# Performance work log

Measured on AMD Instinct MI355X. Metric: run time of the kernel, lower is better.

## Reference

```python
import jax, jax.numpy as jnp
import numpy as np

EMBED_DIM = 1024
NUM_HEADS = 16
HEAD_DIM = EMBED_DIM // NUM_HEADS
MAX_REL = 64
B, S = 4, 1024


def setup_inputs() -> dict:
    key = jax.random.key(0)
    ks = jax.random.split(key, 12)
    scale = 1.0 / np.sqrt(EMBED_DIM)
    inp = {
        "query": jax.random.normal(ks[0], (B, S, EMBED_DIM), jnp.float32),
        "key": jax.random.normal(ks[1], (B, S, EMBED_DIM), jnp.float32),
        "value": jax.random.normal(ks[2], (B, S, EMBED_DIM), jnp.float32),
        "attn_mask": jnp.ones((B, 1, S, S), jnp.int32),
        # projection weights stored [in, out] so x @ W matches torch Linear(x) with W = weight.T
        "Wq": jax.random.normal(ks[3], (EMBED_DIM, EMBED_DIM), jnp.float32) * scale,
        "bq": jnp.zeros((EMBED_DIM,), jnp.float32),
        "Wk": jax.random.normal(ks[4], (EMBED_DIM, EMBED_DIM), jnp.float32) * scale,
        "bk": jnp.zeros((EMBED_DIM,), jnp.float32),
        "Wv": jax.random.normal(ks[5], (EMBED_DIM, EMBED_DIM), jnp.float32) * scale,
        "bv": jnp.zeros((EMBED_DIM,), jnp.float32),
        "Wo": jax.random.normal(ks[6], (EMBED_DIM, EMBED_DIM), jnp.float32) * scale,
        "bo": jnp.zeros((EMBED_DIM,), jnp.float32),
        "rel_pos_embed": jax.random.normal(ks[7], (2 * MAX_REL + 1, HEAD_DIM), jnp.float32) * 0.02,
    }
    return inp


def _split_heads(x):
    # [B, S, E] -> [B, H, S, D]
    b, s, _ = x.shape
    return x.reshape(b, s, NUM_HEADS, HEAD_DIM).transpose(0, 2, 1, 3)


def reference(query, key, value, attn_mask, Wq, bq, Wk, bk, Wv, bv, Wo, bo, rel_pos_embed):
    q = _split_heads(query @ Wq + bq)
    k = _split_heads(key @ Wk + bk)
    v = _split_heads(value @ Wv + bv)

    scores = jnp.einsum("bhqd,bhkd->bhqk", q, k) / np.sqrt(HEAD_DIM).astype(np.float32)

    # relative position bias: rel_pos[i, j] = rel_pos_embed[clip(i - j) + MAX_REL]
    seq_len = scores.shape[-1]
    rng = jnp.arange(seq_len)
    range_mat = jnp.clip(rng[:, None] - rng[None, :], -MAX_REL, MAX_REL) + MAX_REL
    rel_pos = rel_pos_embed[range_mat]                       # [S, S, D]
    # torch: matmul(q[...,None,:], rel_pos.mT).squeeze(-2) == einsum over head_dim (NOT scaled)
    rel_scores = jnp.einsum("bhid,ijd->bhij", q, rel_pos)
    scores = scores + rel_scores

    scores = jnp.where(attn_mask == 0, -jnp.inf, scores)
    attn_weights = jax.nn.softmax(scores, axis=-1)           # dropout p=0.0 -> identity

    out = jnp.einsum("bhqk,bhkd->bhqd", attn_weights, v)
    out = out.transpose(0, 2, 1, 3).reshape(query.shape[0], -1, EMBED_DIM)
    out = out @ Wo + bo
    return out, attn_weights
```

## Files before the change

kernel.cpp:

```cpp
#include <hip/hip_runtime.h>
#include <math.h>

#define BB 4
#define SS 1024
#define EE 1024
#define HH 16
#define DD 64
#define RR 129
#define PRELW 130

typedef __attribute__((ext_vector_type(4))) float f32x4;
typedef __attribute__((ext_vector_type(4))) int   i32x4;
typedef __attribute__((ext_vector_type(8))) short bf8;
typedef __attribute__((ext_vector_type(4))) short s4v;

#define MFMA(a, b, c) __builtin_amdgcn_mfma_f32_16x16x32_bf16(a, b, c, 0, 0, 0)

__device__ __forceinline__ float bf2f(unsigned short u) {
    return __uint_as_float(((unsigned)u) << 16);
}
__device__ __forceinline__ unsigned short f2bf(float x) {
    unsigned u = __float_as_uint(x);
    return (unsigned short)((u + 0x7fffu + ((u >> 16) & 1u)) >> 16);
}

__global__ __launch_bounds__(256, 4)
void wtrans_kernel(const float* __restrict__ Wq, const float* __restrict__ Wk,
                   const float* __restrict__ Wv, const float* __restrict__ Wo,
                   unsigned short* __restrict__ wt_hi, unsigned short* __restrict__ wt_lo)
{
    __shared__ float T[64][65];
    const int w = blockIdx.z;
    const float* W = w == 0 ? Wq : (w == 1 ? Wk : (w == 2 ? Wv : Wo));
    const int n0 = blockIdx.x * 64, k0 = blockIdx.y * 64;
    const int tid = threadIdx.x;
#pragma unroll
    for (int i = 0; i < 4; ++i) {
        int c = tid + 256 * i; int r = c >> 4, c4 = c & 15;
        f32x4 v = *(const f32x4*)(W + (size_t)(k0 + r) * EE + n0 + c4 * 4);
        T[r][c4 * 4 + 0] = v.x; T[r][c4 * 4 + 1] = v.y;
        T[r][c4 * 4 + 2] = v.z; T[r][c4 * 4 + 3] = v.w;
    }
    __syncthreads();
#pragma unroll
    for (int i = 0; i < 4; ++i) {
        int c = tid + 256 * i; int r = c >> 4, c4 = c & 15;
        float x0 = T[c4 * 4 + 0][r], x1 = T[c4 * 4 + 1][r];
        float x2 = T[c4 * 4 + 2][r], x3 = T[c4 * 4 + 3][r];
        unsigned short h0 = f2bf(x0), h1 = f2bf(x1), h2 = f2bf(x2), h3 = f2bf(x3);
        unsigned short l0 = f2bf(x0 - bf2f(h0)), l1 = f2bf(x1 - bf2f(h1));
        unsigned short l2 = f2bf(x2 - bf2f(h2)), l3 = f2bf(x3 - bf2f(h3));
        size_t o = (size_t)w * 1048576 + (size_t)(n0 + r) * 1024 + k0 + c4 * 4;
        *(s4v*)&wt_hi[o] = (s4v){(short)h0, (short)h1, (short)h2, (short)h3};
        *(s4v*)&wt_lo[o] = (s4v){(short)l0, (short)l1, (short)l2, (short)l3};
    }
}

__global__ __launch_bounds__(256)
void maskbits_kernel(const int* __restrict__ mask, unsigned long long* __restrict__ mb)
{
    const int w = blockIdx.x * 256 + threadIdx.x;
    const int* p = mask + (size_t)w * 64;
    unsigned long long bits = 0;
#pragma unroll
    for (int i = 0; i < 16; ++i) {
        int4 v = *(const int4*)(p + i * 4);
        bits |= (unsigned long long)(v.x != 0) << (i * 4 + 0);
        bits |= (unsigned long long)(v.y != 0) << (i * 4 + 1);
        bits |= (unsigned long long)(v.z != 0) << (i * 4 + 2);
        bits |= (unsigned long long)(v.w != 0) << (i * 4 + 3);
    }
    mb[w] = bits;
}

template<int ASRC, int EPI>
__device__ __forceinline__ void gemm_body(
    const float* __restrict__ Af,
    const unsigned short* __restrict__ Ah_g, const unsigned short* __restrict__ Al_g,
    const unsigned short* __restrict__ Bh_g, const unsigned short* __restrict__ Bl_g,
    const float* __restrict__ bias,
    float* __restrict__ Yf, unsigned short* __restrict__ Yh, unsigned short* __restrict__ Yl,
    unsigned short* As_h, unsigned short* As_l, unsigned short* Bs_h, unsigned short* Bs_l,
    int m0, int n0)
{
    const int tid = threadIdx.x, lane = tid & 63, wid = tid >> 6;
    const int wm = (wid >> 1) * 64, wn = (wid & 1) * 64;
    f32x4 zero4 = {0.f, 0.f, 0.f, 0.f};
    f32x4 acc[4][4];
#pragma unroll
    for (int a = 0; a < 4; ++a)
#pragma unroll
        for (int b = 0; b < 4; ++b) acc[a][b] = zero4;

    for (int kt = 0; kt < 1024; kt += 64) {
        __syncthreads();
        if (ASRC == 0) {
#pragma unroll
            for (int i = 0; i < 8; ++i) {
                int c = tid + 256 * i; int r = c >> 4, c4 = c & 15;
                f32x4 v = *(const f32x4*)(Af + (size_t)(m0 + r) * 1024 + kt + c4 * 4);
                unsigned short h0 = f2bf(v.x), h1 = f2bf(v.y), h2 = f2bf(v.z), h3 = f2bf(v.w);
                unsigned short l0 = f2bf(v.x - bf2f(h0)), l1 = f2bf(v.y - bf2f(h1));
                unsigned short l2 = f2bf(v.z - bf2f(h2)), l3 = f2bf(v.w - bf2f(h3));
                int off = r * 64 + (((c4 >> 1) ^ (r & 7)) * 8) + (c4 & 1) * 4;
                *(s4v*)&As_h[off] = (s4v){(short)h0, (short)h1, (short)h2, (short)h3};
                *(s4v*)&As_l[off] = (s4v){(short)l0, (short)l1, (short)l2, (short)l3};
            }
        } else {
#pragma unroll
            for (int i = 0; i < 4; ++i) {
                int c = tid + 256 * i; int r = c >> 3, cc = c & 7;
                int off = r * 64 + ((cc ^ (r & 7)) * 8);
                *(bf8*)&As_h[off] = *(const bf8*)(Ah_g + (size_t)(m0 + r) * 1024 + kt + cc * 8);
                *(bf8*)&As_l[off] = *(const bf8*)(Al_g + (size_t)(m0 + r) * 1024 + kt + cc * 8);
            }
        }
#pragma unroll
        for (int i = 0; i < 4; ++i) {
            int c = tid + 256 * i; int r = c >> 3, cc = c & 7;
            int off = r * 64 + ((cc ^ (r & 7)) * 8);
            *(bf8*)&Bs_h[off] = *(const bf8*)(Bh_g + (size_t)(n0 + r) * 1024 + kt + cc * 8);
            *(bf8*)&Bs_l[off] = *(const bf8*)(Bl_g + (size_t)(n0 + r) * 1024 + kt + cc * 8);
        }
        __syncthreads();
#pragma unroll
        for (int ks = 0; ks < 2; ++ks) {
            bf8 ah[4], al[4], bh[4], bl[4];
#pragma unroll
            for (int f = 0; f < 4; ++f) {
                int ra = wm + f * 16 + (lane & 15);
                int ca = (ks * 4 + (lane >> 4)) ^ (ra & 7);
                ah[f] = *(const bf8*)&As_h[ra * 64 + ca * 8];
                al[f] = *(const bf8*)&As_l[ra * 64 + ca * 8];
                int rb = wn + f * 16 + (lane & 15);
                int cb = (ks * 4 + (lane >> 4)) ^ (rb & 7);
                bh[f] = *(const bf8*)&Bs_h[rb * 64 + cb * 8];
                bl[f] = *(const bf8*)&Bs_l[rb * 64 + cb * 8];
            }
#pragma unroll
            for (int fi = 0; fi < 4; ++fi)
#pragma unroll
                for (int fj = 0; fj < 4; ++fj) {
                    acc[fi][fj] = MFMA(ah[fi], bh[fj], acc[fi][fj]);
                    acc[fi][fj] = MFMA(al[fi], bh[fj], acc[fi][fj]);
                    acc[fi][fj] = MFMA(ah[fi], bl[fj], acc[fi][fj]);
                }
        }
    }
#pragma unroll
    for (int fi = 0; fi < 4; ++fi)
#pragma unroll
        for (int fj = 0; fj < 4; ++fj)
#pragma unroll
            for (int rg = 0; rg < 4; ++rg) {
                int m = m0 + wm + fi * 16 + ((lane >> 4) << 2) + rg;
                int n = n0 + wn + fj * 16 + (lane & 15);
                float val = acc[fi][fj][rg] + bias[n];
                if (EPI == 0) {
                    int b = m >> 10, s = m & 1023, h = n >> 6, d = n & 63;
                    size_t o = (((size_t)(b * 16 + h)) * 1024 + s) * 64 + d;
                    unsigned short hv = f2bf(val);
                    unsigned short lv = f2bf(val - bf2f(hv));
                    Yh[o] = hv; Yl[o] = lv;
                } else {
                    Yf[(size_t)m * 1024 + n] = val;
                }
            }
}

__global__ __launch_bounds__(256, 2)
void proj_qkv_kernel(const float* __restrict__ q_in, const float* __restrict__ k_in,
                     const float* __restrict__ v_in,
                     const unsigned short* __restrict__ wt_hi, const unsigned short* __restrict__ wt_lo,
                     const float* __restrict__ bq, const float* __restrict__ bk,
                     const float* __restrict__ bv,
                     unsigned short* qh_hi, unsigned short* qh_lo,
                     unsigned short* kh_hi, unsigned short* kh_lo,
                     unsigned short* vh_hi, unsigned short* vh_lo)
{
    __shared__ __align__(16) unsigned short As_h[128 * 64], As_l[128 * 64];
    __shared__ __align__(16) unsigned short Bs_h[128 * 64], Bs_l[128 * 64];
    const int z = blockIdx.z;
    const float* X = z == 0 ? q_in : (z == 1 ? k_in : v_in);
    const float* bias = z == 0 ? bq : (z == 1 ? bk : bv);
    unsigned short* Yh = z == 0 ? qh_hi : (z == 1 ? kh_hi : vh_hi);
    unsigned short* Yl = z == 0 ? qh_lo : (z == 1 ? kh_lo : vh_lo);
    gemm_body<0, 0>(X, nullptr, nullptr,
                    wt_hi + (size_t)z * 1048576, wt_lo + (size_t)z * 1048576,
                    bias, nullptr, Yh, Yl, As_h, As_l, Bs_h, Bs_l,
                    blockIdx.x * 128, blockIdx.y * 128);
}

__global__ __launch_bounds__(256, 2)
void outproj_kernel(const unsigned short* __restrict__ ctx_hi, const unsigned short* __restrict__ ctx_lo,
                    const unsigned short* __restrict__ wo_hi, const unsigned short* __restrict__ wo_lo,
                    const float* __restrict__ bo, float* __restrict__ out)
{
    __shared__ __align__(16) unsigned short As_h[128 * 64], As_l[128 * 64];
    __shared__ __align__(16) unsigned short Bs_h[128 * 64], Bs_l[128 * 64];
    gemm_body<1, 1>(nullptr, ctx_hi, ctx_lo, wo_hi, wo_lo, bo, out, nullptr, nullptr,
                    As_h, As_l, Bs_h, Bs_l, blockIdx.x * 128, blockIdx.y * 128);
}

__global__ __launch_bounds__(256, 4)
void vtrans_kernel(const unsigned short* __restrict__ vh_hi, const unsigned short* __restrict__ vh_lo,
                   unsigned short* __restrict__ vt_hi, unsigned short* __restrict__ vt_lo)
{
    __shared__ unsigned short T[64][72];
    const unsigned short* src = blockIdx.z ? vh_lo : vh_hi;
    unsigned short* dst = blockIdx.z ? vt_lo : vt_hi;
    const int st = blockIdx.x * 64, bh = blockIdx.y, tid = threadIdx.x;
#pragma unroll
    for (int i = 0; i < 4; ++i) {
        int c = tid + 256 * i; int r = c >> 4, d4 = c & 15;
        s4v v = *(const s4v*)(src + ((size_t)bh * 1024 + st + r) * 64 + d4 * 4);
        T[r][d4 * 4 + 0] = (unsigned short)v.x; T[r][d4 * 4 + 1] = (unsigned short)v.y;
        T[r][d4 * 4 + 2] = (unsigned short)v.z; T[r][d4 * 4 + 3] = (unsigned short)v.w;
    }
    __syncthreads();
#pragma unroll
    for (int i = 0; i < 4; ++i) {
        int c = tid + 256 * i; int r = c >> 4, s4_ = c & 15;
        s4v o = {(short)T[s4_ * 4 + 0][r], (short)T[s4_ * 4 + 1][r],
                 (short)T[s4_ * 4 + 2][r], (short)T[s4_ * 4 + 3][r]};
        *(s4v*)(dst + ((size_t)bh * 64 + r) * 1024 + st + s4_ * 4) = o;
    }
}

__global__ __launch_bounds__(256, 2)
void attn_fused_kernel(const unsigned short* __restrict__ qh_hi, const unsigned short* __restrict__ qh_lo,
                       const unsigned short* __restrict__ kh_hi, const unsigned short* __restrict__ kh_lo,
                       const unsigned short* __restrict__ vt_hi, const unsigned short* __restrict__ vt_lo,
                       const float* __restrict__ emb, const unsigned long long* __restrict__ mb,
                       float* __restrict__ attn,
                       unsigned short* __restrict__ ctx_hi, unsigned short* __restrict__ ctx_lo)
{
    __shared__ __align__(16) unsigned short Sh[128 * 64], Sl[128 * 64];
    __shared__ __align__(16) unsigned short Pr[128 * PRELW];
    __shared__ float Sm[2][128], Ss[2][128], SmF[128], SsF[128];
    const int tid = threadIdx.x, lane = tid & 63, wid = tid >> 6;
    const int wi = wid >> 1, wj = wid & 1;
    const int g = lane >> 4, li = lane & 15;
    const int bh = blockIdx.x, i0 = blockIdx.y * 128, b = bh >> 4;
    const f32x4 zero4 = {0.f, 0.f, 0.f, 0.f};

    const unsigned short* qbh = qh_hi + ((size_t)bh * 1024 + i0) * 64;
    const unsigned short* qbl = qh_lo + ((size_t)bh * 1024 + i0) * 64;
#pragma unroll
    for (int i = 0; i < 4; ++i) {
        int c = tid + 256 * i; int r = c >> 3, cc = c & 7;
        int off = r * 64 + ((cc ^ (r & 7)) * 8);
        *(bf8*)&Sh[off] = *(const bf8*)(qbh + r * 64 + cc * 8);
        *(bf8*)&Sl[off] = *(const bf8*)(qbl + r * 64 + cc * 8);
    }
    __syncthreads();

    bf8 qfh[4][2], qfl[4][2];
#pragma unroll
    for (int fi = 0; fi < 4; ++fi)
#pragma unroll
        for (int ks = 0; ks < 2; ++ks) {
            int rb = wi * 64 + fi * 16 + li;
            int cb = (ks * 4 + g) ^ (rb & 7);
            qfh[fi][ks] = *(const bf8*)&Sh[rb * 64 + cb * 8];
            qfl[fi][ks] = *(const bf8*)&Sl[rb * 64 + cb * 8];
        }

    for (int t = wid; t < 72; t += 4) {
        const int it = t / 9, rt = t % 9;
        f32x4 pc = zero4;
#pragma unroll
        for (int ks = 0; ks < 2; ++ks) {
            int ra = it * 16 + li;
            int ca = (ks * 4 + g) ^ (ra & 7);
            bf8 aq = *(const bf8*)&Sh[ra * 64 + ca * 8];
            int er = rt * 16 + li; if (er > 128) er = 128;
            const float* ep = emb + (size_t)er * 64 + ks * 32 + g * 8;
            f32x4 e0 = *(const f32x4*)ep;
            f32x4 e1 = *(const f32x4*)(ep + 4);
            bf8 be = {(short)f2bf(e0.x), (short)f2bf(e0.y), (short)f2bf(e0.z), (short)f2bf(e0.w),
                      (short)f2bf(e1.x), (short)f2bf(e1.y), (short)f2bf(e1.z), (short)f2bf(e1.w)};
            pc = MFMA(aq, be, pc);
        }
        const int rcol = rt * 16 + li;
        if (rcol < RR) {
#pragma unroll
            for (int rg = 0; rg < 4; ++rg)
                Pr[(it * 16 + g * 4 + rg) * PRELW + rcol] = f2bf(pc[rg]);
        }
    }

    float rm[4], rs[4];
#pragma unroll
    for (int i = 0; i < 4; ++i) { rm[i] = -3.0e38f; rs[i] = 0.f; }

    for (int jt = 0; jt < 8; ++jt) {
        __syncthreads();
        const unsigned short* kbh = kh_hi + ((size_t)bh * 1024 + jt * 128) * 64;
        const unsigned short* kbl = kh_lo + ((size_t)bh * 1024 + jt * 128) * 64;
#pragma unroll
        for (int i = 0; i < 4; ++i) {
            int c = tid + 256 * i; int r = c >> 3, cc = c & 7;
            int off = r * 64 + ((cc ^ (r & 7)) * 8);
            *(bf8*)&Sh[off] = *(const bf8*)(kbh + r * 64 + cc * 8);
            *(bf8*)&Sl[off] = *(const bf8*)(kbl + r * 64 + cc * 8);
        }
        __syncthreads();
        f32x4 acc[4][4];
#pragma unroll
        for (int a = 0; a < 4; ++a)
#pragma unroll
            for (int c = 0; c < 4; ++c) acc[a][c] = zero4;
#pragma unroll
        for (int ks = 0; ks < 2; ++ks) {
            bf8 kfh[4], kfl[4];
#pragma unroll
            for (int fj = 0; fj < 4; ++fj) {
                int ra = wj * 64 + fj * 16 + li;
                int ca = (ks * 4 + g) ^ (ra & 7);
                kfh[fj] = *(const bf8*)&Sh[ra * 64 + ca * 8];
                kfl[fj] = *(const bf8*)&Sl[ra * 64 + ca * 8];
            }
#pragma unroll
            for (int fj = 0; fj < 4; ++fj)
#pragma unroll
                for (int fi = 0; fi < 4; ++fi) {
                    acc[fj][fi] = MFMA(kfh[fj], qfh[fi][ks], acc[fj][fi]);
                    acc[fj][fi] = MFMA(kfl[fj], qfh[fi][ks], acc[fj][fi]);
                    acc[fj][fi] = MFMA(kfh[fj], qfl[fi][ks], acc[fj][fi]);
                }
        }
#pragma unroll
        for (int fi = 0; fi < 4; ++fi) {
            const int rowL = wi * 64 + fi * 16 + li;
            const int ii = i0 + rowL;
            const unsigned long long mw = mb[((size_t)b * 1024 + ii) * 16 + jt * 2 + wj];
            float p16[4][4];
            float tmax = -3.0e38f;
#pragma unroll
            for (int fj = 0; fj < 4; ++fj)
#pragma unroll
                for (int rg = 0; rg < 4; ++rg) {
                    int jloc = fj * 16 + g * 4 + rg;
                    int jj = jt * 128 + wj * 64 + jloc;
                    int dd = ii - jj; dd = dd < -64 ? -64 : (dd > 64 ? 64 : dd);
                    float s = acc[fj][fi][rg] * 0.125f + bf2f(Pr[rowL * PRELW + dd + 64]);
                    if (!((mw >> jloc) & 1ull)) s = -1.0e30f;
                    p16[fj][rg] = s;
                    tmax = fmaxf(tmax, s);
                }
            tmax = fmaxf(tmax, __shfl_xor(tmax, 16, 64));
            tmax = fmaxf(tmax, __shfl_xor(tmax, 32, 64));
            float nm = fmaxf(rm[fi], tmax);
            float ps = 0.f;
#pragma unroll
            for (int fj = 0; fj < 4; ++fj)
#pragma unroll
                for (int rg = 0; rg < 4; ++rg) ps += __expf(p16[fj][rg] - nm);
            ps += __shfl_xor(ps, 16, 64);
            ps += __shfl_xor(ps, 32, 64);
            rs[fi] = rs[fi] * __expf(rm[fi] - nm) + ps;
            rm[fi] = nm;
        }
    }
#pragma unroll
    for (int fi = 0; fi < 4; ++fi) {
        if (lane < 16) {
            Sm[wj][wi * 64 + fi * 16 + li] = rm[fi];
            Ss[wj][wi * 64 + fi * 16 + li] = rs[fi];
        }
    }
    __syncthreads();
    if (tid < 128) {
        float m0_ = Sm[0][tid], m1_ = Sm[1][tid];
        float mmx = fmaxf(m0_, m1_);
        SmF[tid] = mmx;
        SsF[tid] = Ss[0][tid] * __expf(m0_ - mmx) + Ss[1][tid] * __expf(m1_ - mmx);
    }
    __syncthreads();
    float mm4[4], iv4[4];
#pragma unroll
    for (int fi = 0; fi < 4; ++fi) {
        mm4[fi] = SmF[wi * 64 + fi * 16 + li];
        iv4[fi] = 1.f / SsF[wi * 64 + fi * 16 + li];
    }

    f32x4 ctx_acc[4][4];
#pragma unroll
    for (int a = 0; a < 4; ++a)
#pragma unroll
        for (int c = 0; c < 4; ++c) ctx_acc[a][c] = zero4;

    for (int jt = 0; jt < 8; ++jt) {
        __syncthreads();
        const unsigned short* kbh = kh_hi + ((size_t)bh * 1024 + jt * 128) * 64;
        const unsigned short* kbl = kh_lo + ((size_t)bh * 1024 + jt * 128) * 64;
#pragma unroll
        for (int i = 0; i < 4; ++i) {
            int c = tid + 256 * i; int r = c >> 3, cc = c & 7;
            int off = r * 64 + ((cc ^ (r & 7)) * 8);
            *(bf8*)&Sh[off] = *(const bf8*)(kbh + r * 64 + cc * 8);
            *(bf8*)&Sl[off] = *(const bf8*)(kbl + r * 64 + cc * 8);
        }
        __syncthreads();
        f32x4 acc[4][4];
#pragma unroll
        for (int a = 0; a < 4; ++a)
#pragma unroll
            for (int c = 0; c < 4; ++c) acc[a][c] = zero4;
#pragma unroll
        for (int ks = 0; ks < 2; ++ks) {
            bf8 kfh[4], kfl[4];
#pragma unroll
            for (int fj = 0; fj < 4; ++fj) {
                int ra = wj * 64 + fj * 16 + li;
                int ca = (ks * 4 + g) ^ (ra & 7);
                kfh[fj] = *(const bf8*)&Sh[ra * 64 + ca * 8];
                kfl[fj] = *(const bf8*)&Sl[ra * 64 + ca * 8];
            }
#pragma unroll
            for (int fj = 0; fj < 4; ++fj)
#pragma unroll
                for (int fi = 0; fi < 4; ++fi) {
                    acc[fj][fi] = MFMA(kfh[fj], qfh[fi][ks], acc[fj][fi]);
                    acc[fj][fi] = MFMA(kfl[fj], qfh[fi][ks], acc[fj][fi]);
                    acc[fj][fi] = MFMA(kfh[fj], qfl[fi][ks], acc[fj][fi]);
                }
        }
#pragma unroll
        for (int c = 0; c < 2; ++c) {
            bf8 vfh[4], vfl[4];
#pragma unroll
            for (int fd = 0; fd < 4; ++fd) {
                size_t vb = (size_t)bh * 65536 + (size_t)(fd * 16 + li) * 1024
                          + jt * 128 + wj * 64 + c * 32 + g * 8;
                vfh[fd] = *(const bf8*)(vt_hi + vb);
                vfl[fd] = *(const bf8*)(vt_lo + vb);
            }
#pragma unroll
            for (int fi = 0; fi < 4; ++fi) {
                const int rowL = wi * 64 + fi * 16 + li;
                const int ii = i0 + rowL;
                const unsigned long long mw = mb[((size_t)b * 1024 + ii) * 16 + jt * 2 + wj];
                const float mmf = mm4[fi], ivf = iv4[fi];
                float* arow = attn + ((size_t)bh * 1024 + ii) * 1024 + jt * 128 + wj * 64 + g * 4;
                unsigned wh[2][2], wl[2][2];
#pragma unroll
                for (int t = 0; t < 2; ++t) {
                    const int fj = c * 2 + t;
                    f32x4 pv;
#pragma unroll
                    for (int rg = 0; rg < 4; ++rg) {
                        int jloc = fj * 16 + g * 4 + rg;
                        int jj = jt * 128 + wj * 64 + jloc;
                        int dd = ii - jj; dd = dd < -64 ? -64 : (dd > 64 ? 64 : dd);
                        float s = acc[fj][fi][rg] * 0.125f + bf2f(Pr[rowL * PRELW + dd + 64]);
                        if (!((mw >> jloc) & 1ull)) s = -1.0e30f;
                        pv[rg] = __expf(s - mmf) * ivf;
                    }
                    __builtin_nontemporal_store(pv, (f32x4*)(arow + fj * 16));
                    unsigned short h0 = f2bf(pv.x), h1 = f2bf(pv.y), h2 = f2bf(pv.z), h3 = f2bf(pv.w);
                    wh[t][0] = (unsigned)h0 | ((unsigned)h1 << 16);
                    wh[t][1] = (unsigned)h2 | ((unsigned)h3 << 16);
                    unsigned short l0 = f2bf(pv.x - bf2f(h0)), l1 = f2bf(pv.y - bf2f(h1));
                    unsigned short l2 = f2bf(pv.z - bf2f(h2)), l3 = f2bf(pv.w - bf2f(h3));
                    wl[t][0] = (unsigned)l0 | ((unsigned)l1 << 16);
                    wl[t][1] = (unsigned)l2 | ((unsigned)l3 << 16);
                }
                const int src0 = ((g & 1) * 2) * 16 + li;
                const int src1 = src0 + 16;
                const bool hiT = (g >> 1) & 1;
                int x0A = __shfl((int)wh[0][0], src0, 64), x0B = __shfl((int)wh[1][0], src0, 64);
                int x1A = __shfl((int)wh[0][1], src0, 64), x1B = __shfl((int)wh[1][1], src0, 64);
                int x2A = __shfl((int)wh[0][0], src1, 64), x2B = __shfl((int)wh[1][0], src1, 64);
                int x3A = __shfl((int)wh[0][1], src1, 64), x3B = __shfl((int)wh[1][1], src1, 64);
                i32x4 awh = {hiT ? x0B : x0A, hiT ? x1B : x1A, hiT ? x2B : x2A, hiT ? x3B : x3A};
                bf8 pah = *(bf8*)&awh;
                int y0A = __shfl((int)wl[0][0], src0, 64), y0B = __shfl((int)wl[1][0], src0, 64);
                int y1A = __shfl((int)wl[0][1], src0, 64), y1B = __shfl((int)wl[1][1], src0, 64);
                int y2A = __shfl((int)wl[0][0], src1, 64), y2B = __shfl((int)wl[1][0], src1, 64);
                int y3A = __shfl((int)wl[0][1], src1, 64), y3B = __shfl((int)wl[1][1], src1, 64);
                i32x4 awl = {hiT ? y0B : y0A, hiT ? y1B : y1A, hiT ? y2B : y2A, hiT ? y3B : y3A};
                bf8 pal = *(bf8*)&awl;
#pragma unroll
                for (int fd = 0; fd < 4; ++fd) {
                    ctx_acc[fi][fd] = MFMA(pah, vfh[fd], ctx_acc[fi][fd]);
                    ctx_acc[fi][fd] = MFMA(pal, vfh[fd], ctx_acc[fi][fd]);
                    ctx_acc[fi][fd] = MFMA(pah, vfl[fd], ctx_acc[fi][fd]);
                }
            }
        }
    }

    __syncthreads();
    float* red = (wi == 0) ? (float*)Sh : (float*)Sl;
    if (wj == 1) {
#pragma unroll
        for (int fi = 0; fi < 4; ++fi)
#pragma unroll
            for (int fd = 0; fd < 4; ++fd)
#pragma unroll
                for (int rg = 0; rg < 4; ++rg) {
                    int idx = (fi * 4 + fd) * 4 + rg;
                    red[lane * 64 + ((idx + lane) & 63)] = ctx_acc[fi][fd][rg];
                }
    }
    __syncthreads();
    if (wj == 0) {
        const int b_ = bh >> 4, h = bh & 15;
#pragma unroll
        for (int fi = 0; fi < 4; ++fi)
#pragma unroll
            for (int fd = 0; fd < 4; ++fd)
#pragma unroll
                for (int rg = 0; rg < 4; ++rg) {
                    int idx = (fi * 4 + fd) * 4 + rg;
                    float val = ctx_acc[fi][fd][rg] + red[lane * 64 + ((idx + lane) & 63)];
                    int ii = i0 + wi * 64 + fi * 16 + g * 4 + rg;
                    int d = fd * 16 + li;
                    size_t o = ((size_t)b_ * 1024 + ii) * 1024 + h * 64 + d;
                    unsigned short hv = f2bf(val);
                    unsigned short lv = f2bf(val - bf2f(hv));
                    __builtin_nontemporal_store(hv, &ctx_hi[o]);
                    __builtin_nontemporal_store(lv, &ctx_lo[o]);
                }
    }
}

extern "C" void kernel_launch(void* const* d_in, const int* in_sizes, int n_in,
                              void* d_out, int out_size, void* d_ws, size_t ws_size,
                              hipStream_t stream)
{
    const float* query = (const float*)d_in[0];
    const float* key_  = (const float*)d_in[1];
    const float* value = (const float*)d_in[2];
    const int*   mask  = (const int*)d_in[3];
    const float* Wq = (const float*)d_in[4];
    const float* bq = (const float*)d_in[5];
    const float* Wk = (const float*)d_in[6];
    const float* bk = (const float*)d_in[7];
    const float* Wv = (const float*)d_in[8];
    const float* bv = (const float*)d_in[9];
    const float* Wo = (const float*)d_in[10];
    const float* bo = (const float*)d_in[11];
    const float* emb = (const float*)d_in[12];

    unsigned short* wt_hi = (unsigned short*)d_ws;
    unsigned short* wt_lo = wt_hi + (size_t)4 * 1048576;
    unsigned short* qh_hi = wt_lo + (size_t)4 * 1048576;
    unsigned short* qh_lo = qh_hi + 4194304;
    unsigned short* kh_hi = qh_lo + 4194304;
    unsigned short* kh_lo = kh_hi + 4194304;
    unsigned short* vt_hi = kh_lo + 4194304;
    unsigned short* vt_lo = vt_hi + 4194304;
    unsigned short* ctx_hi = vt_lo + 4194304;
    unsigned short* ctx_lo = ctx_hi + 4194304;
    unsigned long long* mb = (unsigned long long*)d_ws;
    unsigned short* vh_hi = (unsigned short*)d_out;
    unsigned short* vh_lo = vh_hi + 4194304;

    float* out  = (float*)d_out;
    float* attn = (float*)d_out + 4194304;

    dim3 blk(256);
    wtrans_kernel<<<dim3(16, 16, 4), blk, 0, stream>>>(Wq, Wk, Wv, Wo, wt_hi, wt_lo);
    proj_qkv_kernel<<<dim3(32, 8, 3), blk, 0, stream>>>(query, key_, value, wt_hi, wt_lo,
                                                        bq, bk, bv, qh_hi, qh_lo,
                                                        kh_hi, kh_lo, vh_hi, vh_lo);
    maskbits_kernel<<<dim3(256), blk, 0, stream>>>(mask, mb);
    vtrans_kernel<<<dim3(16, 64, 2), blk, 0, stream>>>(vh_hi, vh_lo, vt_hi, vt_lo);
    attn_fused_kernel<<<dim3(64, 8), blk, 0, stream>>>(qh_hi, qh_lo, kh_hi, kh_lo,
                                                       vt_hi, vt_lo, emb, mb,
                                                       attn, ctx_hi, ctx_lo);
    outproj_kernel<<<dim3(32, 8), blk, 0, stream>>>(ctx_hi, ctx_lo,
                                                    wt_hi + (size_t)3 * 1048576,
                                                    wt_lo + (size_t)3 * 1048576, bo, out);
}
```

Measured before the change: 482.3 us.

## Write V transposed from projection epilogue and load Q/K tiles via global_load_lds

The QKV projection epilogue now writes V directly in [b,h,d,s] layout, which removes the separate V transpose kernel and its round trip through memory. The Q/K tile staging in the attention kernel uses direct global-to-LDS loads with the XOR swizzle applied on the global address side, so data no longer passes through registers. The transposed epilogue stores are strided by 1024 elements and poorly coalesced. The LDS-direct loads depend on the per-lane destination layout matching the swizzle the reads expect.

```diff
diff --git a/kernel.cpp b/kernel.cpp
--- a/kernel.cpp
+++ b/kernel.cpp
@@ -22,6 +22,13 @@
 __device__ __forceinline__ unsigned short f2bf(float x) {
     unsigned u = __float_as_uint(x);
     return (unsigned short)((u + 0x7fffu + ((u >> 16) & 1u)) >> 16);
+}
+
+__device__ __forceinline__ void glds16(const unsigned short* g, unsigned short* l) {
+    __builtin_amdgcn_global_load_lds(
+        (const __attribute__((address_space(1))) void*)g,
+        (__attribute__((address_space(3))) void*)l,
+        16, 0, 0);
 }
 
 __global__ __launch_bounds__(256, 4)
@@ -81,7 +88,7 @@
     const float* __restrict__ bias,
     float* __restrict__ Yf, unsigned short* __restrict__ Yh, unsigned short* __restrict__ Yl,
     unsigned short* As_h, unsigned short* As_l, unsigned short* Bs_h, unsigned short* Bs_l,
-    int m0, int n0)
+    int m0, int n0, int vt_out)
 {
     const int tid = threadIdx.x, lane = tid & 63, wid = tid >> 6;
     const int wm = (wid >> 1) * 64, wn = (wid & 1) * 64;
@@ -158,7 +165,9 @@
                 float val = acc[fi][fj][rg] + bias[n];
                 if (EPI == 0) {
                     int b = m >> 10, s = m & 1023, h = n >> 6, d = n & 63;
-                    size_t o = (((size_t)(b * 16 + h)) * 1024 + s) * 64 + d;
+                    size_t o = vt_out
+                        ? (((size_t)(b * 16 + h)) * 64 + d) * 1024 + s
+                        : (((size_t)(b * 16 + h)) * 1024 + s) * 64 + d;
                     unsigned short hv = f2bf(val);
                     unsigned short lv = f2bf(val - bf2f(hv));
                     Yh[o] = hv; Yl[o] = lv;
@@ -176,19 +185,19 @@
                      const float* __restrict__ bv,
                      unsigned short* qh_hi, unsigned short* qh_lo,
                      unsigned short* kh_hi, unsigned short* kh_lo,
-                     unsigned short* vh_hi, unsigned short* vh_lo)
+                     unsigned short* vt_hi, unsigned short* vt_lo)
 {
     __shared__ __align__(16) unsigned short As_h[128 * 64], As_l[128 * 64];
     __shared__ __align__(16) unsigned short Bs_h[128 * 64], Bs_l[128 * 64];
     const int z = blockIdx.z;
     const float* X = z == 0 ? q_in : (z == 1 ? k_in : v_in);
     const float* bias = z == 0 ? bq : (z == 1 ? bk : bv);
-    unsigned short* Yh = z == 0 ? qh_hi : (z == 1 ? kh_hi : vh_hi);
-    unsigned short* Yl = z == 0 ? qh_lo : (z == 1 ? kh_lo : vh_lo);
+    unsigned short* Yh = z == 0 ? qh_hi : (z == 1 ? kh_hi : vt_hi);
+    unsigned short* Yl = z == 0 ? qh_lo : (z == 1 ? kh_lo : vt_lo);
     gemm_body<0, 0>(X, nullptr, nullptr,
                     wt_hi + (size_t)z * 1048576, wt_lo + (size_t)z * 1048576,
                     bias, nullptr, Yh, Yl, As_h, As_l, Bs_h, Bs_l,
-                    blockIdx.x * 128, blockIdx.y * 128);
+                    blockIdx.x * 128, blockIdx.y * 128, z == 2 ? 1 : 0);
 }
 
 __global__ __launch_bounds__(256, 2)
@@ -199,32 +208,7 @@
     __shared__ __align__(16) unsigned short As_h[128 * 64], As_l[128 * 64];
     __shared__ __align__(16) unsigned short Bs_h[128 * 64], Bs_l[128 * 64];
     gemm_body<1, 1>(nullptr, ctx_hi, ctx_lo, wo_hi, wo_lo, bo, out, nullptr, nullptr,
-                    As_h, As_l, Bs_h, Bs_l, blockIdx.x * 128, blockIdx.y * 128);
-}
-
-__global__ __launch_bounds__(256, 4)
-void vtrans_kernel(const unsigned short* __restrict__ vh_hi, const unsigned short* __restrict__ vh_lo,
-                   unsigned short* __restrict__ vt_hi, unsigned short* __restrict__ vt_lo)
-{
-    __shared__ unsigned short T[64][72];
-    const unsigned short* src = blockIdx.z ? vh_lo : vh_hi;
-    unsigned short* dst = blockIdx.z ? vt_lo : vt_hi;
-    const int st = blockIdx.x * 64, bh = blockIdx.y, tid = threadIdx.x;
-#pragma unroll
-    for (int i = 0; i < 4; ++i) {
-        int c = tid + 256 * i; int r = c >> 4, d4 = c & 15;
-        s4v v = *(const s4v*)(src + ((size_t)bh * 1024 + st + r) * 64 + d4 * 4);
-        T[r][d4 * 4 + 0] = (unsigned short)v.x; T[r][d4 * 4 + 1] = (unsigned short)v.y;
-        T[r][d4 * 4 + 2] = (unsigned short)v.z; T[r][d4 * 4 + 3] = (unsigned short)v.w;
-    }
-    __syncthreads();
-#pragma unroll
-    for (int i = 0; i < 4; ++i) {
-        int c = tid + 256 * i; int r = c >> 4, s4_ = c & 15;
-        s4v o = {(short)T[s4_ * 4 + 0][r], (short)T[s4_ * 4 + 1][r],
-                 (short)T[s4_ * 4 + 2][r], (short)T[s4_ * 4 + 3][r]};
-        *(s4v*)(dst + ((size_t)bh * 64 + r) * 1024 + st + s4_ * 4) = o;
-    }
+                    As_h, As_l, Bs_h, Bs_l, blockIdx.x * 128, blockIdx.y * 128, 0);
 }
 
 __global__ __launch_bounds__(256, 2)
@@ -244,14 +228,19 @@
     const int bh = blockIdx.x, i0 = blockIdx.y * 128, b = bh >> 4;
     const f32x4 zero4 = {0.f, 0.f, 0.f, 0.f};
 
+    int sr_[4], sc_[4];
+#pragma unroll
+    for (int i = 0; i < 4; ++i) {
+        sr_[i] = (wid * 4 + i) * 8 + (lane >> 3);
+        sc_[i] = (lane & 7) ^ (sr_[i] & 7);
+    }
+
     const unsigned short* qbh = qh_hi + ((size_t)bh * 1024 + i0) * 64;
     const unsigned short* qbl = qh_lo + ((size_t)bh * 1024 + i0) * 64;
 #pragma unroll
     for (int i = 0; i < 4; ++i) {
-        int c = tid + 256 * i; int r = c >> 3, cc = c & 7;
-        int off = r * 64 + ((cc ^ (r & 7)) * 8);
-        *(bf8*)&Sh[off] = *(const bf8*)(qbh + r * 64 + cc * 8);
-        *(bf8*)&Sl[off] = *(const bf8*)(qbl + r * 64 + cc * 8);
+        glds16(qbh + sr_[i] * 64 + sc_[i] * 8, Sh + (size_t)(wid * 4 + i) * 512);
+        glds16(qbl + sr_[i] * 64 + sc_[i] * 8, Sl + (size_t)(wid * 4 + i) * 512);
     }
     __syncthreads();
 
@@ -300,10 +289,8 @@
         const unsigned short* kbl = kh_lo + ((size_t)bh * 1024 + jt * 128) * 64;
 #pragma unroll
         for (int i = 0; i < 4; ++i) {
-            int c = tid + 256 * i; int r = c >> 3, cc = c & 7;
-            int off = r * 64 + ((cc ^ (r & 7)) * 8);
-            *(bf8*)&Sh[off] = *(const bf8*)(kbh + r * 64 + cc * 8);
-            *(bf8*)&Sl[off] = *(const bf8*)(kbl + r * 64 + cc * 8);
+            glds16(kbh + sr_[i] * 64 + sc_[i] * 8, Sh + (size_t)(wid * 4 + i) * 512);
+            glds16(kbl + sr_[i] * 64 + sc_[i] * 8, Sl + (size_t)(wid * 4 + i) * 512);
         }
         __syncthreads();
         f32x4 acc[4][4];
@@ -397,10 +384,8 @@
         const unsigned short* kbl = kh_lo + ((size_t)bh * 1024 + jt * 128) * 64;
 #pragma unroll
         for (int i = 0; i < 4; ++i) {
-            int c = tid + 256 * i; int r = c >> 3, cc = c & 7;
-            int off = r * 64 + ((cc ^ (r & 7)) * 8);
-            *(bf8*)&Sh[off] = *(const bf8*)(kbh + r * 64 + cc * 8);
-            *(bf8*)&Sl[off] = *(const bf8*)(kbl + r * 64 + cc * 8);
+            glds16(kbh + sr_[i] * 64 + sc_[i] * 8, Sh + (size_t)(wid * 4 + i) * 512);
+            glds16(kbl + sr_[i] * 64 + sc_[i] * 8, Sl + (size_t)(wid * 4 + i) * 512);
         }
         __syncthreads();
         f32x4 acc[4][4];
@@ -556,8 +541,6 @@
     unsigned short* ctx_hi = vt_lo + 4194304;
     unsigned short* ctx_lo = ctx_hi + 4194304;
     unsigned long long* mb = (unsigned long long*)d_ws;
-    unsigned short* vh_hi = (unsigned short*)d_out;
-    unsigned short* vh_lo = vh_hi + 4194304;
 
     float* out  = (float*)d_out;
     float* attn = (float*)d_out + 4194304;
@@ -566,9 +549,8 @@
     wtrans_kernel<<<dim3(16, 16, 4), blk, 0, stream>>>(Wq, Wk, Wv, Wo, wt_hi, wt_lo);
     proj_qkv_kernel<<<dim3(32, 8, 3), blk, 0, stream>>>(query, key_, value, wt_hi, wt_lo,
                                                         bq, bk, bv, qh_hi, qh_lo,
-                                                        kh_hi, kh_lo, vh_hi, vh_lo);
+                                                        kh_hi, kh_lo, vt_hi, vt_lo);
     maskbits_kernel<<<dim3(256), blk, 0, stream>>>(mask, mb);
-    vtrans_kernel<<<dim3(16, 64, 2), blk, 0, stream>>>(vh_hi, vh_lo, vt_hi, vt_lo);
     attn_fused_kernel<<<dim3(64, 8), blk, 0, stream>>>(qh_hi, qh_lo, kh_hi, kh_lo,
                                                        vt_hi, vt_lo, emb, mb,
                                                        attn, ctx_hi, ctx_lo);
```

Result: faster. 466.2 us (-3.3%).
